# Kernel tuning notes

Measured on AMD Instinct MI355X. Metric: run time of the kernel, lower is better.

The kernel has to match this reference:

```python
import jax, jax.numpy as jnp
import numpy as np

C = 256


def _conv1x1(x, w, b):
    # x: [B,C,H,W], w: [O,C], b: [O] -> 1x1 conv == per-pixel linear
    return jnp.einsum('bchw,oc->bohw', x, w) + b[None, :, None, None]


def setup_inputs() -> dict:
    key = jax.random.key(0)
    ks = jax.random.split(key, 10)
    B, H, W = 4, 64, 64
    scale = 1.0 / np.sqrt(C)
    inp = {
        'F_c': jax.random.normal(ks[0], (B, C, H, W), jnp.float32),
        'F_s': jax.random.normal(ks[1], (B, C, H, W), jnp.float32),
        'w_f': jax.random.normal(ks[2], (C, C), jnp.float32) * scale,
        'b_f': jax.random.normal(ks[3], (C,), jnp.float32) * 0.01,
        'w_g': jax.random.normal(ks[4], (C, C), jnp.float32) * scale,
        'b_g': jax.random.normal(ks[5], (C,), jnp.float32) * 0.01,
        'w_h': jax.random.normal(ks[6], (C, C), jnp.float32) * scale,
        'b_h': jax.random.normal(ks[7], (C,), jnp.float32) * 0.01,
        'w_o': jax.random.normal(ks[8], (C, C), jnp.float32) * scale,
        'b_o': jax.random.normal(ks[9], (C,), jnp.float32) * 0.01,
    }
    return inp


def reference(F_c, F_s, w_f, b_f, w_g, b_g, w_h, b_h, w_o, b_o):
    b, c, h, w = F_c.shape
    Fq = _conv1x1(F_c, w_f, b_f).reshape(b, c, -1)   # [B,C,Nq]
    G = _conv1x1(F_s, w_g, b_g).reshape(b, c, -1)    # [B,C,Nk]
    Hv = _conv1x1(F_s, w_h, b_h).reshape(b, c, -1)   # [B,C,Nk]
    # S[b,i,j] = sum_c Fq[b,c,i] * G[b,c,j]; softmax over keys j
    S = jax.nn.softmax(jnp.einsum('bci,bcj->bij', Fq, G), axis=-1)
    # result[b,c,i] = sum_j Hv[b,c,j] * S[b,i,j]
    res = jnp.einsum('bcj,bij->bci', Hv, S).reshape(b, c, h, w)
    return _conv1x1(res, w_o, b_o)
```

## Files before the change

kernel.cpp:

```cpp
#include <hip/hip_runtime.h>
#include <hip/hip_bf16.h>

typedef __attribute__((ext_vector_type(8))) short bf16x8;
typedef __attribute__((ext_vector_type(4))) float f32x4;
typedef __attribute__((ext_vector_type(8))) _Float16 f16x8;
typedef __attribute__((ext_vector_type(8))) unsigned short u16x8;
typedef unsigned int uint32;
typedef unsigned short ushort;

#define MFMA16(a, b, c) __builtin_amdgcn_mfma_f32_16x16x32_bf16((a), (b), (c), 0, 0, 0)

__device__ __forceinline__ ushort f2bf(float f) {
    __hip_bfloat16 h = __float2bfloat16(f);
    return __builtin_bit_cast(ushort, h);
}
__device__ __forceinline__ float bf2f(ushort u) {
    uint32 v = ((uint32)u) << 16;
    return __builtin_bit_cast(float, v);
}
__device__ __forceinline__ void gld16(const ushort* g, ushort* l) {
    __builtin_amdgcn_global_load_lds(
        (const __attribute__((address_space(1))) unsigned int*)g,
        (__attribute__((address_space(3))) unsigned int*)l, 16, 0, 0);
}

__global__ __launch_bounds__(256) void transpose_split(
    const float* __restrict__ Fc, const float* __restrict__ Fs,
    ushort* __restrict__ XcH, ushort* __restrict__ XcL,
    ushort* __restrict__ XsH, ushort* __restrict__ XsL) {
    __shared__ float lds[64][65];
    const int z = blockIdx.z;
    const int b = z & 3;
    const float* src = (z < 4) ? Fc : Fs;
    ushort* dh = (z < 4) ? XcH : XsH;
    ushort* dl = (z < 4) ? XcL : XsL;
    src += (size_t)b * 256 * 4096;
    dh += (size_t)b * 4096 * 256;
    dl += (size_t)b * 4096 * 256;
    const int i0 = blockIdx.x * 64;
    const int c0 = blockIdx.y * 64;
    const int col = threadIdx.x & 63;
    const int rb = threadIdx.x >> 6;
#pragma unroll
    for (int rr = 0; rr < 16; rr++) {
        int r = rb * 16 + rr;
        lds[r][col] = src[(size_t)(c0 + r) * 4096 + i0 + col];
    }
    __syncthreads();
#pragma unroll
    for (int rr = 0; rr < 16; rr++) {
        int r = rb * 16 + rr;
        float f = lds[col][r];
        ushort h = f2bf(f);
        dh[(size_t)(i0 + r) * 256 + c0 + col] = h;
        dl[(size_t)(i0 + r) * 256 + c0 + col] = f2bf(f - bf2f(h));
    }
}

__global__ __launch_bounds__(256) void convert_weights(
    const float* __restrict__ wf, const float* __restrict__ wg,
    const float* __restrict__ wh, const float* __restrict__ wo,
    ushort* __restrict__ wfh, ushort* __restrict__ wfl,
    ushort* __restrict__ wgh, ushort* __restrict__ wgl,
    ushort* __restrict__ whb, ushort* __restrict__ wob) {
    const int t = blockIdx.x * 256 + threadIdx.x;
    const float L2E = 1.4426950408889634f;
    float sf = wf[t] * L2E;
    ushort hf = f2bf(sf);
    wfh[t] = hf;
    wfl[t] = f2bf(sf - bf2f(hf));
    float sg = wg[t];
    ushort hg = f2bf(sg);
    wgh[t] = hg;
    wgl[t] = f2bf(sg - bf2f(hg));
    whb[t] = f2bf(wh[t]);
    wob[t] = f2bf(wo[t]);
}

__global__ __launch_bounds__(256) void proj_qk(
    const ushort* __restrict__ XcH, const ushort* __restrict__ XcL,
    const ushort* __restrict__ XsH, const ushort* __restrict__ XsL,
    const ushort* __restrict__ wfh, const ushort* __restrict__ wfl,
    const ushort* __restrict__ wgh, const ushort* __restrict__ wgl,
    const float* __restrict__ bf_, const float* __restrict__ bg_,
    ushort* __restrict__ QH, ushort* __restrict__ QL,
    ushort* __restrict__ KH, ushort* __restrict__ KL) {
    const int y = blockIdx.y;
    const int isK = y >> 2;
    const int b = y & 3;
    const size_t bNC = (size_t)b * 4096 * 256;
    const ushort* Ah = (isK ? XsH : XcH) + bNC;
    const ushort* Al = (isK ? XsL : XcL) + bNC;
    const ushort* Bh = isK ? wgh : wfh;
    const ushort* Bl = isK ? wgl : wfl;
    const float* bias = isK ? bg_ : bf_;
    const float bscale = isK ? 1.0f : 1.4426950408889634f;
    ushort* Ch = (isK ? KH : QH) + bNC;
    ushort* Cl = (isK ? KL : QL) + bNC;
    const int m0 = (blockIdx.x & 63) * 64, n0 = (blockIdx.x >> 6) * 64;
    const int l = threadIdx.x & 63, wv = threadIdx.x >> 6;
    const int g = l >> 4, l15 = l & 15;
    const int mrow = m0 + wv * 16 + l15;

    f32x4 acc[4] = {{0, 0, 0, 0}, {0, 0, 0, 0}, {0, 0, 0, 0}, {0, 0, 0, 0}};
#pragma unroll
    for (int kk = 0; kk < 8; kk++) {
        bf16x8 ah = *(const bf16x8*)(Ah + (size_t)mrow * 256 + kk * 32 + g * 8);
        bf16x8 al = *(const bf16x8*)(Al + (size_t)mrow * 256 + kk * 32 + g * 8);
#pragma unroll
        for (int nt = 0; nt < 4; nt++) {
            const size_t boff = (size_t)(n0 + nt * 16 + l15) * 256 + kk * 32 + g * 8;
            bf16x8 bh = *(const bf16x8*)(Bh + boff);
            bf16x8 bl = *(const bf16x8*)(Bl + boff);
            acc[nt] = MFMA16(ah, bh, acc[nt]);
            acc[nt] = MFMA16(ah, bl, acc[nt]);
            acc[nt] = MFMA16(al, bh, acc[nt]);
        }
    }
#pragma unroll
    for (int nt = 0; nt < 4; nt++) {
        float bn = bias[n0 + nt * 16 + l15] * bscale;
#pragma unroll
        for (int r = 0; r < 4; r++) {
            int mr = m0 + wv * 16 + g * 4 + r;
            float v = acc[nt][r] + bn;
            ushort h = f2bf(v);
            Ch[(size_t)mr * 256 + n0 + nt * 16 + l15] = h;
            Cl[(size_t)mr * 256 + n0 + nt * 16 + l15] = f2bf(v - bf2f(h));
        }
    }
}

__global__ __launch_bounds__(256) void proj_v(
    const ushort* __restrict__ XsH, const ushort* __restrict__ whb,
    const float* __restrict__ bh_, ushort* __restrict__ Vv) {
    const int b = blockIdx.y;
    const size_t bNC = (size_t)b * 4096 * 256;
    const ushort* A = whb;
    const ushort* Bp = XsH + bNC;
    ushort* Cp = Vv + bNC;
    const int m0 = (blockIdx.x & 3) * 64, n0 = (blockIdx.x >> 2) * 64;
    const int l = threadIdx.x & 63, wv = threadIdx.x >> 6;
    const int g = l >> 4, l15 = l & 15;
    const int mrow = m0 + wv * 16 + l15;

    f32x4 acc[4] = {{0, 0, 0, 0}, {0, 0, 0, 0}, {0, 0, 0, 0}, {0, 0, 0, 0}};
#pragma unroll
    for (int kk = 0; kk < 8; kk++) {
        bf16x8 af = *(const bf16x8*)(A + (size_t)mrow * 256 + kk * 32 + g * 8);
#pragma unroll
        for (int nt = 0; nt < 4; nt++) {
            bf16x8 bfr = *(const bf16x8*)(Bp + (size_t)(n0 + nt * 16 + l15) * 256 + kk * 32 + g * 8);
            acc[nt] = MFMA16(af, bfr, acc[nt]);
        }
    }
#pragma unroll
    for (int nt = 0; nt < 4; nt++) {
#pragma unroll
        for (int r = 0; r < 4; r++) {
            int mr = m0 + wv * 16 + g * 4 + r;
            Cp[(size_t)mr * 4096 + n0 + nt * 16 + l15] = f2bf(acc[nt][r] + bh_[mr]);
        }
    }
}

__global__ __launch_bounds__(512, 2) void attn_split(
    const ushort* __restrict__ QH, const ushort* __restrict__ QL,
    const ushort* __restrict__ KH, const ushort* __restrict__ KL,
    const ushort* __restrict__ Vv, _Float16* __restrict__ Opart,
    float2* __restrict__ ML) {
    __shared__ __align__(16) ushort Khi[32 * 256];
    __shared__ __align__(16) ushort Klo[32 * 256];
    __shared__ __align__(16) ushort Vt[256 * 32];

    const int h = blockIdx.x;
    const int xcd = h & 7;
    const int j = h >> 3;
    const int grp = xcd + 8 * (j & 1);
    const int itile = j >> 1;
    const int b = grp >> 2;
    const int s = grp & 3;

    const int l = threadIdx.x & 63, wv = threadIdx.x >> 6;
    const int g = l >> 4, l15 = l & 15;
    const int iw = itile * 128 + wv * 16;
    const ushort* QHb = QH + ((size_t)b * 4096 + iw) * 256;
    const ushort* QLb = QL + ((size_t)b * 4096 + iw) * 256;
    const ushort* KHb = KH + (size_t)b * 4096 * 256;
    const ushort* KLb = KL + (size_t)b * 4096 * 256;
    const ushort* Vb = Vv + (size_t)b * 4096 * 256;

    bf16x8 qh[8], ql[8];
#pragma unroll
    for (int kk = 0; kk < 8; kk++) {
        qh[kk] = *(const bf16x8*)(QHb + (size_t)l15 * 256 + kk * 32 + g * 8);
        ql[kk] = *(const bf16x8*)(QLb + (size_t)l15 * 256 + kk * 32 + g * 8);
    }

    f32x4 acc[16];
#pragma unroll
    for (int ct = 0; ct < 16; ct++) acc[ct] = (f32x4){0, 0, 0, 0};
    float M = -INFINITY, Lsum = 0.0f;

    const int r0 = l15, r1 = l15 + 16;
    const int jbeg = s * 1024, jend = jbeg + 1024;
    for (int j0 = jbeg; j0 < jend; j0 += 32) {
        {
            const ushort* khs = KHb + (size_t)j0 * 256;
            const ushort* kls = KLb + (size_t)j0 * 256;
#pragma unroll
            for (int q = 0; q < 2; q++) {
                int issue = wv * 2 + q;
                int row = issue * 2 + (l >> 5);
                int scol = (((l & 31) ^ row) & 31) * 8;
                gld16(khs + (size_t)row * 256 + scol, &Khi[issue * 512]);
                gld16(kls + (size_t)row * 256 + scol, &Klo[issue * 512]);
                int ch = issue * 16 + (l >> 2);
                gld16(Vb + (size_t)ch * 4096 + j0 + (l & 3) * 8, &Vt[issue * 512]);
            }
        }
        asm volatile("s_waitcnt vmcnt(0)" ::: "memory");
        __syncthreads();

        f32x4 s0a = {0, 0, 0, 0}, s0b = {0, 0, 0, 0}, s0c = {0, 0, 0, 0};
        f32x4 s1a = {0, 0, 0, 0}, s1b = {0, 0, 0, 0}, s1c = {0, 0, 0, 0};
#pragma unroll
        for (int kk = 0; kk < 8; kk++) {
            const int cs = kk * 4 + g;
            bf16x8 kh0 = *(const bf16x8*)&Khi[r0 * 256 + ((cs ^ r0) & 31) * 8];
            bf16x8 kl0 = *(const bf16x8*)&Klo[r0 * 256 + ((cs ^ r0) & 31) * 8];
            bf16x8 kh1 = *(const bf16x8*)&Khi[r1 * 256 + ((cs ^ r1) & 31) * 8];
            bf16x8 kl1 = *(const bf16x8*)&Klo[r1 * 256 + ((cs ^ r1) & 31) * 8];
            s0a = MFMA16(kh0, qh[kk], s0a);
            s0b = MFMA16(kh0, ql[kk], s0b);
            s0c = MFMA16(kl0, qh[kk], s0c);
            s1a = MFMA16(kh1, qh[kk], s1a);
            s1b = MFMA16(kh1, ql[kk], s1b);
            s1c = MFMA16(kl1, qh[kk], s1c);
        }
        f32x4 s0 = (s0a + s0b) + s0c;
        f32x4 s1 = (s1a + s1b) + s1c;
        float tm = fmaxf(fmaxf(fmaxf(s0[0], s0[1]), fmaxf(s0[2], s0[3])),
                         fmaxf(fmaxf(s1[0], s1[1]), fmaxf(s1[2], s1[3])));
        tm = fmaxf(tm, __shfl_xor(tm, 16));
        tm = fmaxf(tm, __shfl_xor(tm, 32));
        float newM = fmaxf(M, tm);
        if (__any(newM > M)) {
            float alpha = exp2f(M - newM);
            Lsum *= alpha;
            float ar[4];
#pragma unroll
            for (int r = 0; r < 4; r++) ar[r] = __shfl(alpha, g * 4 + r);
#pragma unroll
            for (int ct = 0; ct < 16; ct++) {
#pragma unroll
                for (int r = 0; r < 4; r++) acc[ct][r] *= ar[r];
            }
        }
        M = newM;
        float p[8];
#pragma unroll
        for (int r = 0; r < 4; r++) {
            p[r] = exp2f(s0[r] - M);
            p[4 + r] = exp2f(s1[r] - M);
        }
        Lsum += p[0] + p[1] + p[2] + p[3] + p[4] + p[5] + p[6] + p[7];

        uint32 pk[4];
        pk[0] = (uint32)f2bf(p[0]) | ((uint32)f2bf(p[1]) << 16);
        pk[1] = (uint32)f2bf(p[2]) | ((uint32)f2bf(p[3]) << 16);
        pk[2] = (uint32)f2bf(p[4]) | ((uint32)f2bf(p[5]) << 16);
        pk[3] = (uint32)f2bf(p[6]) | ((uint32)f2bf(p[7]) << 16);
        const int ts = g >> 1;
        const int s1l = l15 + ((g & 1) << 5);
        uint32 w0a = __shfl(pk[0], s1l), w0b = __shfl(pk[2], s1l);
        uint32 w1a = __shfl(pk[1], s1l), w1b = __shfl(pk[3], s1l);
        uint32 w2a = __shfl(pk[0], s1l + 16), w2b = __shfl(pk[2], s1l + 16);
        uint32 w3a = __shfl(pk[1], s1l + 16), w3b = __shfl(pk[3], s1l + 16);
        union { uint32 u[4]; bf16x8 v; } pun;
        pun.u[0] = ts ? w0b : w0a;
        pun.u[1] = ts ? w1b : w1a;
        pun.u[2] = ts ? w2b : w2a;
        pun.u[3] = ts ? w3b : w3a;
        bf16x8 pf = pun.v;

#pragma unroll
        for (int ct = 0; ct < 16; ct++) {
            bf16x8 vf = *(const bf16x8*)&Vt[(ct * 16 + l15) * 32 + g * 8];
            acc[ct] = MFMA16(pf, vf, acc[ct]);
        }
        __syncthreads();
    }
    float Lt = Lsum + __shfl_xor(Lsum, 16);
    Lt += __shfl_xor(Lt, 32);
    float inv = 1.0f / Lt;
    float ivr[4];
#pragma unroll
    for (int r = 0; r < 4; r++) ivr[r] = __shfl(inv, g * 4 + r);
    const size_t sb = (size_t)(s * 4 + b);
    _Float16* Ob = Opart + (sb * 4096 + iw) * 256;
#pragma unroll
    for (int ct = 0; ct < 16; ct++) {
#pragma unroll
        for (int r = 0; r < 4; r++)
            Ob[(size_t)(g * 4 + r) * 256 + ct * 16 + l15] =
                (_Float16)(acc[ct][r] * ivr[r]);
    }
    if (g == 0) {
        float2 ml;
        ml.x = M;
        ml.y = Lt;
        ML[sb * 4096 + iw + l15] = ml;
    }
}

__global__ __launch_bounds__(256) void attn_combine(
    const _Float16* __restrict__ Opart, const float2* __restrict__ ML,
    ushort* __restrict__ Rt) {
    const int b = blockIdx.y;
    const int i = blockIdx.x * 8 + (threadIdx.x >> 5);
    const int c0 = (threadIdx.x & 31) * 8;
    float m[4], lv[4];
#pragma unroll
    for (int s = 0; s < 4; s++) {
        float2 ml = ML[(size_t)(s * 4 + b) * 4096 + i];
        m[s] = ml.x;
        lv[s] = ml.y;
    }
    float Mmax = fmaxf(fmaxf(m[0], m[1]), fmaxf(m[2], m[3]));
    float w[4], denom = 0.0f;
#pragma unroll
    for (int s = 0; s < 4; s++) {
        w[s] = lv[s] * exp2f(m[s] - Mmax);
        denom += w[s];
    }
    float inv = 1.0f / denom;
    float o[8] = {0, 0, 0, 0, 0, 0, 0, 0};
#pragma unroll
    for (int s = 0; s < 4; s++) {
        float ws = w[s] * inv;
        f16x8 v = *(const f16x8*)(Opart + ((size_t)(s * 4 + b) * 4096 + i) * 256 + c0);
#pragma unroll
        for (int e = 0; e < 8; e++) o[e] += ws * (float)v[e];
    }
    u16x8 r;
#pragma unroll
    for (int e = 0; e < 8; e++) r[e] = f2bf(o[e]);
    *(u16x8*)(Rt + ((size_t)b * 4096 + i) * 256 + c0) = r;
}

__global__ __launch_bounds__(256) void out_proj(
    const ushort* __restrict__ wob, const ushort* __restrict__ Rt,
    const float* __restrict__ bo, float* __restrict__ Out) {
    const int b = blockIdx.y;
    const int m0 = (blockIdx.x & 3) * 64;
    const int n0 = (blockIdx.x >> 2) * 64;
    const int l = threadIdx.x & 63, wv = threadIdx.x >> 6;
    const int g = l >> 4, l15 = l & 15;
    const ushort* Bp = Rt + (size_t)b * 4096 * 256;
    float* Ob = Out + (size_t)b * 256 * 4096;
    const int mrow = m0 + wv * 16 + l15;

    f32x4 acc[4] = {{0, 0, 0, 0}, {0, 0, 0, 0}, {0, 0, 0, 0}, {0, 0, 0, 0}};
#pragma unroll
    for (int kk = 0; kk < 8; kk++) {
        bf16x8 af = *(const bf16x8*)(wob + (size_t)mrow * 256 + kk * 32 + g * 8);
#pragma unroll
        for (int nt = 0; nt < 4; nt++) {
            bf16x8 bfr = *(const bf16x8*)(Bp + (size_t)(n0 + nt * 16 + l15) * 256 + kk * 32 + g * 8);
            acc[nt] = MFMA16(af, bfr, acc[nt]);
        }
    }
#pragma unroll
    for (int nt = 0; nt < 4; nt++) {
#pragma unroll
        for (int r = 0; r < 4; r++) {
            int mr = m0 + wv * 16 + g * 4 + r;
            Ob[(size_t)mr * 4096 + n0 + nt * 16 + l15] = acc[nt][r] + bo[mr];
        }
    }
}

extern "C" void kernel_launch(void* const* d_in, const int* in_sizes, int n_in,
                              void* d_out, int out_size, void* d_ws, size_t ws_size,
                              hipStream_t stream) {
    const float* Fc = (const float*)d_in[0];
    const float* Fs = (const float*)d_in[1];
    const float* wf = (const float*)d_in[2];
    const float* bf_ = (const float*)d_in[3];
    const float* wg = (const float*)d_in[4];
    const float* bg = (const float*)d_in[5];
    const float* wh = (const float*)d_in[6];
    const float* bh = (const float*)d_in[7];
    const float* wo = (const float*)d_in[8];
    const float* bo = (const float*)d_in[9];
    float* Out = (float*)d_out;

    char* ws = (char*)d_ws;
    const size_t SZ = (size_t)4 * 4096 * 256 * 2;
    ushort* QHp = (ushort*)(ws + 0 * SZ);
    ushort* QLp = (ushort*)(ws + 1 * SZ);
    ushort* KHp = (ushort*)(ws + 2 * SZ);
    ushort* KLp = (ushort*)(ws + 3 * SZ);
    ushort* Vv  = (ushort*)(ws + 4 * SZ);
    ushort* XcH = (ushort*)(ws + 5 * SZ);
    ushort* XcL = (ushort*)(ws + 6 * SZ);
    ushort* XsH = (ushort*)(ws + 7 * SZ);
    ushort* XsL = (ushort*)(ws + 8 * SZ);
    _Float16* Opart = (_Float16*)(ws + 5 * SZ);
    char* wsw = ws + 9 * SZ;
    ushort* wfh = (ushort*)(wsw + 0 * 131072);
    ushort* wfl = (ushort*)(wsw + 1 * 131072);
    ushort* wgh = (ushort*)(wsw + 2 * 131072);
    ushort* wgl = (ushort*)(wsw + 3 * 131072);
    ushort* whb = (ushort*)(wsw + 4 * 131072);
    ushort* wob = (ushort*)(wsw + 5 * 131072);
    float2* ML = (float2*)(wsw + 6 * 131072);
    ushort* Rt = QHp;

    transpose_split<<<dim3(64, 4, 8), 256, 0, stream>>>(Fc, Fs, XcH, XcL, XsH, XsL);
    convert_weights<<<dim3(256), 256, 0, stream>>>(wf, wg, wh, wo, wfh, wfl, wgh, wgl, whb, wob);
    proj_qk<<<dim3(256, 8), 256, 0, stream>>>(XcH, XcL, XsH, XsL, wfh, wfl, wgh, wgl,
                                              bf_, bg, QHp, QLp, KHp, KLp);
    proj_v<<<dim3(256, 4), 256, 0, stream>>>(XsH, whb, bh, Vv);
    attn_split<<<dim3(512), 512, 0, stream>>>(QHp, QLp, KHp, KLp, Vv, Opart, ML);
    attn_combine<<<dim3(512, 4), 256, 0, stream>>>(Opart, ML, Rt);
    out_proj<<<dim3(256, 4), 256, 0, stream>>>(wob, Rt, bo, Out);
}
```

Baseline: 408.7 us.

## Use fp16 Q/K in attention with double-buffered K/V and lazy rescale

Q and K are now stored as a single fp16 tensor each instead of bf16 hi/lo pairs, so QK^T drops from three bf16 MFMAs to one fp16 MFMA and K staging traffic is halved. The attention kernel double-buffers K (async global-to-LDS) and V (register prefetch into padded LDS), which removes the per-tile wait before compute. It halves the key split to 2 with 256 blocks, skips rescaling unless the running max grows by more than 8, and the transpose kernel is vectorised. The risks are fp16 precision and range for the logits, lower occupancy from the smaller grid, and possible overflow from the deferred max update.

```diff
diff --git a/kernel.cpp b/kernel.cpp
--- a/kernel.cpp
+++ b/kernel.cpp
@@ -5,10 +5,12 @@
 typedef __attribute__((ext_vector_type(4))) float f32x4;
 typedef __attribute__((ext_vector_type(8))) _Float16 f16x8;
 typedef __attribute__((ext_vector_type(8))) unsigned short u16x8;
+typedef __attribute__((ext_vector_type(4))) unsigned short u16x4;
 typedef unsigned int uint32;
 typedef unsigned short ushort;
 
 #define MFMA16(a, b, c) __builtin_amdgcn_mfma_f32_16x16x32_bf16((a), (b), (c), 0, 0, 0)
+#define MFMA16F(a, b, c) __builtin_amdgcn_mfma_f32_16x16x32_f16((a), (b), (c), 0, 0, 0)
 
 __device__ __forceinline__ ushort f2bf(float f) {
     __hip_bfloat16 h = __float2bfloat16(f);
@@ -39,21 +41,32 @@
     dl += (size_t)b * 4096 * 256;
     const int i0 = blockIdx.x * 64;
     const int c0 = blockIdx.y * 64;
-    const int col = threadIdx.x & 63;
-    const int rb = threadIdx.x >> 6;
-#pragma unroll
-    for (int rr = 0; rr < 16; rr++) {
-        int r = rb * 16 + rr;
-        lds[r][col] = src[(size_t)(c0 + r) * 4096 + i0 + col];
+    const int t = threadIdx.x;
+    const int rq = t >> 4;
+    const int q4 = (t & 15) * 4;
+#pragma unroll
+    for (int p = 0; p < 4; p++) {
+        int r = rq + p * 16;
+        float4 v = *(const float4*)(src + (size_t)(c0 + r) * 4096 + i0 + q4);
+        lds[q4 + 0][r] = v.x;
+        lds[q4 + 1][r] = v.y;
+        lds[q4 + 2][r] = v.z;
+        lds[q4 + 3][r] = v.w;
     }
     __syncthreads();
 #pragma unroll
-    for (int rr = 0; rr < 16; rr++) {
-        int r = rb * 16 + rr;
-        float f = lds[col][r];
-        ushort h = f2bf(f);
-        dh[(size_t)(i0 + r) * 256 + c0 + col] = h;
-        dl[(size_t)(i0 + r) * 256 + c0 + col] = f2bf(f - bf2f(h));
+    for (int p = 0; p < 4; p++) {
+        int i = rq + p * 16;
+        u16x4 hv, lv;
+#pragma unroll
+        for (int e = 0; e < 4; e++) {
+            float f = lds[i][q4 + e];
+            ushort hb = f2bf(f);
+            hv[e] = hb;
+            lv[e] = f2bf(f - bf2f(hb));
+        }
+        *(u16x4*)(dh + (size_t)(i0 + i) * 256 + c0 + q4) = hv;
+        *(u16x4*)(dl + (size_t)(i0 + i) * 256 + c0 + q4) = lv;
     }
 }
 
@@ -83,8 +96,7 @@
     const ushort* __restrict__ wfh, const ushort* __restrict__ wfl,
     const ushort* __restrict__ wgh, const ushort* __restrict__ wgl,
     const float* __restrict__ bf_, const float* __restrict__ bg_,
-    ushort* __restrict__ QH, ushort* __restrict__ QL,
-    ushort* __restrict__ KH, ushort* __restrict__ KL) {
+    _Float16* __restrict__ QF, _Float16* __restrict__ KF) {
     const int y = blockIdx.y;
     const int isK = y >> 2;
     const int b = y & 3;
@@ -95,8 +107,7 @@
     const ushort* Bl = isK ? wgl : wfl;
     const float* bias = isK ? bg_ : bf_;
     const float bscale = isK ? 1.0f : 1.4426950408889634f;
-    ushort* Ch = (isK ? KH : QH) + bNC;
-    ushort* Cl = (isK ? KL : QL) + bNC;
+    _Float16* Co = (isK ? KF : QF) + bNC;
     const int m0 = (blockIdx.x & 63) * 64, n0 = (blockIdx.x >> 6) * 64;
     const int l = threadIdx.x & 63, wv = threadIdx.x >> 6;
     const int g = l >> 4, l15 = l & 15;
@@ -123,10 +134,7 @@
 #pragma unroll
         for (int r = 0; r < 4; r++) {
             int mr = m0 + wv * 16 + g * 4 + r;
-            float v = acc[nt][r] + bn;
-            ushort h = f2bf(v);
-            Ch[(size_t)mr * 256 + n0 + nt * 16 + l15] = h;
-            Cl[(size_t)mr * 256 + n0 + nt * 16 + l15] = f2bf(v - bf2f(h));
+            Co[(size_t)mr * 256 + n0 + nt * 16 + l15] = (_Float16)(acc[nt][r] + bn);
         }
     }
 }
@@ -165,87 +173,101 @@
 }
 
 __global__ __launch_bounds__(512, 2) void attn_split(
-    const ushort* __restrict__ QH, const ushort* __restrict__ QL,
-    const ushort* __restrict__ KH, const ushort* __restrict__ KL,
+    const _Float16* __restrict__ QF, const _Float16* __restrict__ KF,
     const ushort* __restrict__ Vv, _Float16* __restrict__ Opart,
     float2* __restrict__ ML) {
-    __shared__ __align__(16) ushort Khi[32 * 256];
-    __shared__ __align__(16) ushort Klo[32 * 256];
-    __shared__ __align__(16) ushort Vt[256 * 32];
+    __shared__ __align__(16) _Float16 Kf[2][32 * 256];
+    __shared__ __align__(16) ushort Vt[2][256 * 40];
 
     const int h = blockIdx.x;
-    const int xcd = h & 7;
-    const int j = h >> 3;
-    const int grp = xcd + 8 * (j & 1);
-    const int itile = j >> 1;
-    const int b = grp >> 2;
-    const int s = grp & 3;
-
-    const int l = threadIdx.x & 63, wv = threadIdx.x >> 6;
+    const int grp = h & 7;
+    const int itile = h >> 3;
+    const int b = grp >> 1;
+    const int s = grp & 1;
+
+    const int tid = threadIdx.x;
+    const int l = tid & 63, wv = tid >> 6;
     const int g = l >> 4, l15 = l & 15;
     const int iw = itile * 128 + wv * 16;
-    const ushort* QHb = QH + ((size_t)b * 4096 + iw) * 256;
-    const ushort* QLb = QL + ((size_t)b * 4096 + iw) * 256;
-    const ushort* KHb = KH + (size_t)b * 4096 * 256;
-    const ushort* KLb = KL + (size_t)b * 4096 * 256;
+    const _Float16* Qb = QF + ((size_t)b * 4096 + iw) * 256;
+    const _Float16* Kb = KF + (size_t)b * 4096 * 256;
     const ushort* Vb = Vv + (size_t)b * 4096 * 256;
 
-    bf16x8 qh[8], ql[8];
-#pragma unroll
-    for (int kk = 0; kk < 8; kk++) {
-        qh[kk] = *(const bf16x8*)(QHb + (size_t)l15 * 256 + kk * 32 + g * 8);
-        ql[kk] = *(const bf16x8*)(QLb + (size_t)l15 * 256 + kk * 32 + g * 8);
-    }
+    f16x8 qf[8];
+#pragma unroll
+    for (int kk = 0; kk < 8; kk++)
+        qf[kk] = *(const f16x8*)(Qb + (size_t)l15 * 256 + kk * 32 + g * 8);
+
+    const int vch = tid >> 1;
+    const int vko = (tid & 1) * 16;
+    const ushort* Vsrc = Vb + (size_t)vch * 4096;
 
     f32x4 acc[16];
 #pragma unroll
     for (int ct = 0; ct < 16; ct++) acc[ct] = (f32x4){0, 0, 0, 0};
     float M = -INFINITY, Lsum = 0.0f;
 
-    const int r0 = l15, r1 = l15 + 16;
-    const int jbeg = s * 1024, jend = jbeg + 1024;
+    const int jbeg = s * 2048, jend = jbeg + 2048;
+
+    auto stageK = [&](int buf, int jj) {
+        const _Float16* ks = Kb + (size_t)jj * 256;
+#pragma unroll
+        for (int q = 0; q < 2; q++) {
+            int issue = wv * 2 + q;
+            int row = issue * 2 + (l >> 5);
+            int scol = ((l & 31) ^ row) * 8;
+            gld16((const ushort*)(ks + (size_t)row * 256 + scol),
+                  (ushort*)&Kf[buf][issue * 512]);
+        }
+    };
+
+    stageK(0, jbeg);
+    {
+        u16x8 va = *(const u16x8*)(Vsrc + jbeg + vko);
+        u16x8 vb2 = *(const u16x8*)(Vsrc + jbeg + vko + 8);
+        asm volatile("s_waitcnt vmcnt(0)" ::: "memory");
+        *(u16x8*)&Vt[0][vch * 40 + vko] = va;
+        *(u16x8*)&Vt[0][vch * 40 + vko + 8] = vb2;
+    }
+    __syncthreads();
+
+    int cur = 0;
     for (int j0 = jbeg; j0 < jend; j0 += 32) {
-        {
-            const ushort* khs = KHb + (size_t)j0 * 256;
-            const ushort* kls = KLb + (size_t)j0 * 256;
-#pragma unroll
-            for (int q = 0; q < 2; q++) {
-                int issue = wv * 2 + q;
-                int row = issue * 2 + (l >> 5);
-                int scol = (((l & 31) ^ row) & 31) * 8;
-                gld16(khs + (size_t)row * 256 + scol, &Khi[issue * 512]);
-                gld16(kls + (size_t)row * 256 + scol, &Klo[issue * 512]);
-                int ch = issue * 16 + (l >> 2);
-                gld16(Vb + (size_t)ch * 4096 + j0 + (l & 3) * 8, &Vt[issue * 512]);
+        const bool pre = (j0 + 32) < jend;
+        u16x8 va, vb2;
+        if (pre) {
+            stageK(cur ^ 1, j0 + 32);
+            va = *(const u16x8*)(Vsrc + (j0 + 32) + vko);
+            vb2 = *(const u16x8*)(Vsrc + (j0 + 32) + vko + 8);
+        }
+        f32x4 s0e = {0, 0, 0, 0}, s0o = {0, 0, 0, 0};
+        f32x4 s1e = {0, 0, 0, 0}, s1o = {0, 0, 0, 0};
+        const int r1 = l15 + 16;
+#pragma unroll
+        for (int kk = 0; kk < 8; kk += 2) {
+            {
+                int cs = kk * 4 + g;
+                f16x8 k0 = *(const f16x8*)&Kf[cur][l15 * 256 + ((cs ^ l15) & 31) * 8];
+                f16x8 k1 = *(const f16x8*)&Kf[cur][r1 * 256 + ((cs ^ r1) & 31) * 8];
+                s0e = MFMA16F(k0, qf[kk], s0e);
+                s1e = MFMA16F(k1, qf[kk], s1e);
             }
-        }
-        asm volatile("s_waitcnt vmcnt(0)" ::: "memory");
-        __syncthreads();
-
-        f32x4 s0a = {0, 0, 0, 0}, s0b = {0, 0, 0, 0}, s0c = {0, 0, 0, 0};
-        f32x4 s1a = {0, 0, 0, 0}, s1b = {0, 0, 0, 0}, s1c = {0, 0, 0, 0};
-#pragma unroll
-        for (int kk = 0; kk < 8; kk++) {
-            const int cs = kk * 4 + g;
-            bf16x8 kh0 = *(const bf16x8*)&Khi[r0 * 256 + ((cs ^ r0) & 31) * 8];
-            bf16x8 kl0 = *(const bf16x8*)&Klo[r0 * 256 + ((cs ^ r0) & 31) * 8];
-            bf16x8 kh1 = *(const bf16x8*)&Khi[r1 * 256 + ((cs ^ r1) & 31) * 8];
-            bf16x8 kl1 = *(const bf16x8*)&Klo[r1 * 256 + ((cs ^ r1) & 31) * 8];
-            s0a = MFMA16(kh0, qh[kk], s0a);
-            s0b = MFMA16(kh0, ql[kk], s0b);
-            s0c = MFMA16(kl0, qh[kk], s0c);
-            s1a = MFMA16(kh1, qh[kk], s1a);
-            s1b = MFMA16(kh1, ql[kk], s1b);
-            s1c = MFMA16(kl1, qh[kk], s1c);
-        }
-        f32x4 s0 = (s0a + s0b) + s0c;
-        f32x4 s1 = (s1a + s1b) + s1c;
+            {
+                int cs = (kk + 1) * 4 + g;
+                f16x8 k0 = *(const f16x8*)&Kf[cur][l15 * 256 + ((cs ^ l15) & 31) * 8];
+                f16x8 k1 = *(const f16x8*)&Kf[cur][r1 * 256 + ((cs ^ r1) & 31) * 8];
+                s0o = MFMA16F(k0, qf[kk + 1], s0o);
+                s1o = MFMA16F(k1, qf[kk + 1], s1o);
+            }
+        }
+        f32x4 s0 = s0e + s0o;
+        f32x4 s1 = s1e + s1o;
         float tm = fmaxf(fmaxf(fmaxf(s0[0], s0[1]), fmaxf(s0[2], s0[3])),
                          fmaxf(fmaxf(s1[0], s1[1]), fmaxf(s1[2], s1[3])));
         tm = fmaxf(tm, __shfl_xor(tm, 16));
         tm = fmaxf(tm, __shfl_xor(tm, 32));
-        float newM = fmaxf(M, tm);
-        if (__any(newM > M)) {
+        if (__any(tm - M > 8.0f)) {
+            float newM = fmaxf(M, tm);
             float alpha = exp2f(M - newM);
             Lsum *= alpha;
             float ar[4];
@@ -256,8 +278,8 @@
 #pragma unroll
                 for (int r = 0; r < 4; r++) acc[ct][r] *= ar[r];
             }
-        }
-        M = newM;
+            M = newM;
+        }
         float p[8];
 #pragma unroll
         for (int r = 0; r < 4; r++) {
@@ -286,10 +308,16 @@
 
 #pragma unroll
         for (int ct = 0; ct < 16; ct++) {
-            bf16x8 vf = *(const bf16x8*)&Vt[(ct * 16 + l15) * 32 + g * 8];
+            bf16x8 vf = *(const bf16x8*)&Vt[cur][(ct * 16 + l15) * 40 + g * 8];
             acc[ct] = MFMA16(pf, vf, acc[ct]);
         }
+        if (pre) {
+            asm volatile("s_waitcnt vmcnt(0)" ::: "memory");
+            *(u16x8*)&Vt[cur ^ 1][vch * 40 + vko] = va;
+            *(u16x8*)&Vt[cur ^ 1][vch * 40 + vko + 8] = vb2;
+        }
         __syncthreads();
+        cur ^= 1;
     }
     float Lt = Lsum + __shfl_xor(Lsum, 16);
     Lt += __shfl_xor(Lt, 32);
@@ -320,32 +348,19 @@
     const int b = blockIdx.y;
     const int i = blockIdx.x * 8 + (threadIdx.x >> 5);
     const int c0 = (threadIdx.x & 31) * 8;
-    float m[4], lv[4];
-#pragma unroll
-    for (int s = 0; s < 4; s++) {
-        float2 ml = ML[(size_t)(s * 4 + b) * 4096 + i];
-        m[s] = ml.x;
-        lv[s] = ml.y;
-    }
-    float Mmax = fmaxf(fmaxf(m[0], m[1]), fmaxf(m[2], m[3]));
-    float w[4], denom = 0.0f;
-#pragma unroll
-    for (int s = 0; s < 4; s++) {
-        w[s] = lv[s] * exp2f(m[s] - Mmax);
-        denom += w[s];
-    }
-    float inv = 1.0f / denom;
-    float o[8] = {0, 0, 0, 0, 0, 0, 0, 0};
-#pragma unroll
-    for (int s = 0; s < 4; s++) {
-        float ws = w[s] * inv;
-        f16x8 v = *(const f16x8*)(Opart + ((size_t)(s * 4 + b) * 4096 + i) * 256 + c0);
-#pragma unroll
-        for (int e = 0; e < 8; e++) o[e] += ws * (float)v[e];
-    }
+    float2 ml0 = ML[(size_t)(0 * 4 + b) * 4096 + i];
+    float2 ml1 = ML[(size_t)(1 * 4 + b) * 4096 + i];
+    float Mmax = fmaxf(ml0.x, ml1.x);
+    float w0 = ml0.y * exp2f(ml0.x - Mmax);
+    float w1 = ml1.y * exp2f(ml1.x - Mmax);
+    float inv = 1.0f / (w0 + w1);
+    w0 *= inv;
+    w1 *= inv;
+    f16x8 v0 = *(const f16x8*)(Opart + ((size_t)(0 * 4 + b) * 4096 + i) * 256 + c0);
+    f16x8 v1 = *(const f16x8*)(Opart + ((size_t)(1 * 4 + b) * 4096 + i) * 256 + c0);
     u16x8 r;
 #pragma unroll
-    for (int e = 0; e < 8; e++) r[e] = f2bf(o[e]);
+    for (int e = 0; e < 8; e++) r[e] = f2bf(w0 * (float)v0[e] + w1 * (float)v1[e]);
     *(u16x8*)(Rt + ((size_t)b * 4096 + i) * 256 + c0) = r;
 }
 
@@ -398,17 +413,15 @@
 
     char* ws = (char*)d_ws;
     const size_t SZ = (size_t)4 * 4096 * 256 * 2;
-    ushort* QHp = (ushort*)(ws + 0 * SZ);
-    ushort* QLp = (ushort*)(ws + 1 * SZ);
-    ushort* KHp = (ushort*)(ws + 2 * SZ);
-    ushort* KLp = (ushort*)(ws + 3 * SZ);
-    ushort* Vv  = (ushort*)(ws + 4 * SZ);
-    ushort* XcH = (ushort*)(ws + 5 * SZ);
-    ushort* XcL = (ushort*)(ws + 6 * SZ);
-    ushort* XsH = (ushort*)(ws + 7 * SZ);
-    ushort* XsL = (ushort*)(ws + 8 * SZ);
-    _Float16* Opart = (_Float16*)(ws + 5 * SZ);
-    char* wsw = ws + 9 * SZ;
+    _Float16* QFp = (_Float16*)(ws + 0 * SZ);
+    _Float16* KFp = (_Float16*)(ws + 1 * SZ);
+    ushort* Vv  = (ushort*)(ws + 2 * SZ);
+    ushort* XcH = (ushort*)(ws + 3 * SZ);
+    ushort* XcL = (ushort*)(ws + 4 * SZ);
+    ushort* XsH = (ushort*)(ws + 5 * SZ);
+    ushort* XsL = (ushort*)(ws + 6 * SZ);
+    _Float16* Opart = (_Float16*)(ws + 3 * SZ);
+    char* wsw = ws + 7 * SZ;
     ushort* wfh = (ushort*)(wsw + 0 * 131072);
     ushort* wfl = (ushort*)(wsw + 1 * 131072);
     ushort* wgh = (ushort*)(wsw + 2 * 131072);
@@ -416,14 +429,14 @@
     ushort* whb = (ushort*)(wsw + 4 * 131072);
     ushort* wob = (ushort*)(wsw + 5 * 131072);
     float2* ML = (float2*)(wsw + 6 * 131072);
-    ushort* Rt = QHp;
+    ushort* Rt = (ushort*)QFp;
 
     transpose_split<<<dim3(64, 4, 8), 256, 0, stream>>>(Fc, Fs, XcH, XcL, XsH, XsL);
     convert_weights<<<dim3(256), 256, 0, stream>>>(wf, wg, wh, wo, wfh, wfl, wgh, wgl, whb, wob);
     proj_qk<<<dim3(256, 8), 256, 0, stream>>>(XcH, XcL, XsH, XsL, wfh, wfl, wgh, wgl,
-                                              bf_, bg, QHp, QLp, KHp, KLp);
+                                              bf_, bg, QFp, KFp);
     proj_v<<<dim3(256, 4), 256, 0, stream>>>(XsH, whb, bh, Vv);
-    attn_split<<<dim3(512), 512, 0, stream>>>(QHp, QLp, KHp, KLp, Vv, Opart, ML);
+    attn_split<<<dim3(256), 512, 0, stream>>>(QFp, KFp, Vv, Opart, ML);
     attn_combine<<<dim3(512, 4), 256, 0, stream>>>(Opart, ML, Rt);
     out_proj<<<dim3(256, 4), 256, 0, stream>>>(wob, Rt, bo, Out);
 }
```

Result: faster. 352.9 us (-13.7%).
